# Kernel optimization log

Hardware: AMD Instinct MI355X
Metric: run time of the kernel (lower is better)

The kernel has to match this reference:

```python
import jax, jax.numpy as jnp
import numpy as np

N_NODES = 20000
N_EDGES = 200000
D_MODEL = 128
N_HEADS = 8
N_LAYERS = 2  # num_gnn - 1 concat layers


def setup_inputs() -> dict:
    key = jax.random.key(0)
    ks = jax.random.split(key, 12)
    s = 0.05  # keep activations well-scaled across residual layers
    hd = D_MODEL // N_HEADS  # 16
    return {
        "x": jax.random.normal(ks[0], (N_NODES, D_MODEL), jnp.float32),
        "src": jax.random.randint(ks[1], (N_EDGES,), 0, N_NODES),
        "dst": jax.random.randint(ks[2], (N_EDGES,), 0, N_NODES),
        "Ws": jax.random.normal(ks[3], (N_LAYERS, D_MODEL, D_MODEL), jnp.float32) * s,
        "als": jax.random.normal(ks[4], (N_LAYERS, N_HEADS, hd), jnp.float32) * s,
        "ars": jax.random.normal(ks[5], (N_LAYERS, N_HEADS, hd), jnp.float32) * s,
        "bs": jax.random.normal(ks[6], (N_LAYERS, D_MODEL), jnp.float32) * s,
        "W_last": jax.random.normal(ks[7], (D_MODEL, N_HEADS * D_MODEL), jnp.float32) * s,
        "al_last": jax.random.normal(ks[8], (N_HEADS, D_MODEL), jnp.float32) * s,
        "ar_last": jax.random.normal(ks[9], (N_HEADS, D_MODEL), jnp.float32) * s,
        "b_last": jax.random.normal(ks[10], (N_HEADS * D_MODEL,), jnp.float32) * s,
    }


def gat_conv(h, src, dst, W, al, ar, b, num_nodes):
    """DGL GATConv (eval mode, dropout off): returns (N, H, D) head outputs."""
    H, D = al.shape
    feat = (h @ W).reshape(num_nodes, H, D)          # (N,H,D)
    el = jnp.sum(feat * al[None], axis=-1)           # (N,H) attn on src side
    er = jnp.sum(feat * ar[None], axis=-1)           # (N,H) attn on dst side
    e = jax.nn.leaky_relu(el[src] + er[dst], 0.2)    # (E,H)
    # edge softmax over incoming edges of each dst node, per head
    m = jax.ops.segment_max(e, dst, num_segments=num_nodes)  # (N,H)
    p = jnp.exp(e - m[dst])                          # (E,H)
    z = jax.ops.segment_sum(p, dst, num_segments=num_nodes)  # (N,H)
    a = p / z[dst]                                   # (E,H)
    msg = feat[src] * a[..., None]                   # (E,H,D) weighted messages
    rst = jax.ops.segment_sum(msg, dst, num_segments=num_nodes)  # (N,H,D)
    return rst + b.reshape(1, H, D)


def reference(x, src, dst, Ws, als, ars, bs, W_last, al_last, ar_last, b_last):
    N = x.shape[0]
    h = x
    for i in range(N_LAYERS):
        temp = gat_conv(h, src, dst, Ws[i], als[i], ars[i], bs[i], N)  # (N,H,hd)
        h = h + jax.nn.elu(temp.reshape(N, -1))       # concat heads, ELU, residual
    temp = gat_conv(h, src, dst, W_last, al_last, ar_last, b_last, N)  # (N,H,D)
    h = h + jnp.mean(temp, axis=1)                    # mean over heads, residual
    return h
```

## Files before the change

### kernel.cpp

```cpp
#include <hip/hip_runtime.h>
#include <math.h>

#define N_NODES 20000
#define N_EDGES 200000
#define DM 128
#define NH 8

typedef __attribute__((ext_vector_type(8))) short bf16x8;
typedef __attribute__((ext_vector_type(4))) float f32x4;

__device__ __forceinline__ unsigned short f2b(float f) {
  unsigned int u = __float_as_uint(f);
  unsigned int r = (u + 0x7FFFu + ((u >> 16) & 1u)) >> 16;
  return (unsigned short)r;
}
__device__ __forceinline__ float b2f(unsigned short s) {
  return __uint_as_float(((unsigned int)s) << 16);
}

__global__ __launch_bounds__(256) void degzero(int* __restrict__ deg) {
  int i = blockIdx.x * 256 + threadIdx.x;
  if (i < N_NODES) deg[i] = 0;
}

__global__ __launch_bounds__(256) void prep_all(
    const float* __restrict__ x, float* __restrict__ h, unsigned short* __restrict__ hb,
    const int* __restrict__ dstE, int* __restrict__ deg, int* __restrict__ rank,
    const float* __restrict__ Ws, unsigned short* __restrict__ wsz,
    const float* __restrict__ W_last, unsigned short* __restrict__ wpsz,
    const float* __restrict__ al_last, const float* __restrict__ ar_last,
    const float* __restrict__ b_last, unsigned short* __restrict__ wlrsz,
    float* __restrict__ mb) {
  int i = blockIdx.x * 256 + threadIdx.x;
  if (i < (N_NODES * DM) / 4) {
    float4 v = ((const float4*)x)[i];
    ((float4*)h)[i] = v;
    ((ushort4*)hb)[i] = make_ushort4(f2b(v.x), f2b(v.y), f2b(v.z), f2b(v.w));
  }
  if (i < N_EDGES) rank[i] = atomicAdd(&deg[dstE[i]], 1);
  if (i < 2 * 16384) {
    int layer = i >> 14;
    int r = i & 16383;
    int j = r & 7, l = (r >> 3) & 63, f = (r >> 9) & 7, ks = r >> 12;
    int k = ks * 32 + ((l >> 4) << 3) + j;
    int n = f * 16 + (l & 15);
    wsz[i] = f2b(Ws[(size_t)layer * 16384 + k * 128 + n]);
  }
  if (i < 131072) {
    int j = i & 7, l = (i >> 3) & 63, f = (i >> 9) & 7, ks = i >> 12;
    int k = ks * 32 + ((l >> 4) << 3) + j;
    int n = f * 16 + (l & 15);
    int h_ = k >> 7, ko = k & 127;
    wpsz[i] = f2b(W_last[(size_t)ko * 1024 + h_ * 128 + n] * 0.125f);
  }
  if (i < 2048) {
    int j = i & 7, l = (i >> 3) & 63, ks = i >> 9;
    int k = ks * 32 + ((l >> 4) << 3) + j;
    int n = l & 15;
    int hh = n & 7;
    const float* av = (n < 8) ? (al_last + hh * 128) : (ar_last + hh * 128);
    float s = 0.f;
    for (int d = 0; d < 128; ++d) s += W_last[(size_t)k * 1024 + hh * 128 + d] * av[d];
    wlrsz[i] = f2b(s);
  }
  if (i < 128) {
    float s = 0.f;
#pragma unroll
    for (int hh = 0; hh < 8; ++hh) s += b_last[hh * 128 + i];
    mb[i] = s * 0.125f;
  }
}

__global__ void scan_deg(const int* __restrict__ deg, int* __restrict__ off,
                         int* __restrict__ bbase_g, int* __restrict__ bcur_g) {
  __shared__ int part[1024];
  __shared__ int hist[16][64];
  const int tid = threadIdx.x;
  const int wv = tid >> 6, lane = tid & 63;
  const int CHUNK = (N_NODES + 1023) / 1024;
  int base = tid * CHUNK;

  for (int i = tid; i < 16 * 64; i += 1024) ((int*)hist)[i] = 0;
  __syncthreads();

  int s = 0;
  for (int i = 0; i < CHUNK; ++i) {
    int idx = base + i;
    if (idx < N_NODES) {
      int d = deg[idx];
      s += d;
      atomicAdd(&hist[wv][min(d, 63)], 1);
    }
  }
  part[tid] = s;
  __syncthreads();
  for (int ofs = 1; ofs < 1024; ofs <<= 1) {
    int v = (tid >= ofs) ? part[tid - ofs] : 0;
    __syncthreads();
    part[tid] += v;
    __syncthreads();
  }
  int run = (tid > 0) ? part[tid - 1] : 0;
  for (int i = 0; i < CHUNK; ++i) {
    int idx = base + i;
    if (idx < N_NODES) {
      off[idx] = run;
      run += deg[idx];
    }
  }
  if (tid == 0) off[N_NODES] = part[1023];

  if (wv == 0) {
    int c = 0;
#pragma unroll
    for (int w = 0; w < 16; ++w) c += hist[w][lane];
    int inc = c;
#pragma unroll
    for (int ofs = 1; ofs < 64; ofs <<= 1) {
      int v = __shfl_up(inc, ofs, 64);
      if (lane >= ofs) inc += v;
    }
    bbase_g[lane] = inc - c;
    bcur_g[lane] = 0;
  }
}

template <int K>
__device__ __forceinline__ void dev_gemm(int tile, const unsigned short* __restrict__ A,
                                         const unsigned short* __restrict__ Bsz,
                                         unsigned short* __restrict__ Cb,
                                         const float* __restrict__ al,
                                         const float* __restrict__ ar,
                                         float* __restrict__ elr, int lane, int wid) {
  const int wrow = wid & 1, wc = wid >> 1;
  const int r0 = tile * 32;
  const int arow = r0 + wrow * 16 + (lane & 15);
  const int kg = lane >> 4;

  f32x4 acc[4];
#pragma unroll
  for (int fi = 0; fi < 4; ++fi) acc[fi] = {0.f, 0.f, 0.f, 0.f};

  const bf16x8* Ap = (const bf16x8*)(A + (size_t)arow * K + kg * 8);
#pragma unroll 4
  for (int ks = 0; ks < K / 32; ++ks) {
    bf16x8 a = Ap[ks * 4];
#pragma unroll
    for (int fi = 0; fi < 4; ++fi) {
      int f = wc * 4 + fi;
      bf16x8 b = *(const bf16x8*)(Bsz + (((size_t)(ks * 8 + f) * 64 + lane) << 3));
      acc[fi] = __builtin_amdgcn_mfma_f32_16x16x32_bf16(a, b, acc[fi], 0, 0, 0);
    }
  }

  const int rbase = r0 + wrow * 16 + (lane >> 4) * 4;
#pragma unroll
  for (int fi = 0; fi < 4; ++fi) {
    int col = wc * 64 + fi * 16 + (lane & 15);
#pragma unroll
    for (int r = 0; r < 4; ++r) {
      Cb[(size_t)(rbase + r) * DM + col] = f2b(acc[fi][r]);
    }
  }

#pragma unroll
  for (int fi = 0; fi < 4; ++fi) {
    int hh = wc * 4 + fi;
    float alv = al[hh * 16 + (lane & 15)];
    float arv = ar[hh * 16 + (lane & 15)];
#pragma unroll
    for (int r = 0; r < 4; ++r) {
      float pl = acc[fi][r] * alv;
      float pr = acc[fi][r] * arv;
#pragma unroll
      for (int msk = 1; msk < 16; msk <<= 1) {
        pl += __shfl_xor(pl, msk, 64);
        pr += __shfl_xor(pr, msk, 64);
      }
      if ((lane & 15) == 0) {
        int row = rbase + r;
        elr[row * 16 + hh] = pl;
        elr[row * 16 + 8 + hh] = pr;
      }
    }
  }
}

__global__ __launch_bounds__(256) void gemm0_scatter(
    const unsigned short* __restrict__ A, const unsigned short* __restrict__ Bsz,
    unsigned short* __restrict__ Cb, const float* __restrict__ al,
    const float* __restrict__ ar, float* __restrict__ elr, const int* __restrict__ srcE,
    const int* __restrict__ dstE, const int* __restrict__ rank,
    const int* __restrict__ off, int* __restrict__ csr_src, const int* __restrict__ deg,
    const int* __restrict__ bbase_g, int* __restrict__ bcur_g, int* __restrict__ perm) {
  __shared__ int lcnt[64];
  __shared__ int gbase[64];
  const int bid = blockIdx.x;
  const int GB = N_NODES / 32;
  const int EB = (N_EDGES + 255) / 256;
  if (bid < GB) {
    dev_gemm<DM>(bid, A, Bsz, Cb, al, ar, elr, threadIdx.x & 63, threadIdx.x >> 6);
  } else if (bid < GB + EB) {
    int e = (bid - GB) * 256 + threadIdx.x;
    if (e < N_EDGES) {
      csr_src[off[dstE[e]] + rank[e]] = srcE[e];
    }
  } else {
    const int tid = threadIdx.x;
    int idx = (bid - GB - EB) * 256 + tid;
    if (tid < 64) lcnt[tid] = 0;
    __syncthreads();
    int d = 0, lrank = 0;
    bool valid = idx < N_NODES;
    if (valid) {
      d = min(deg[idx], 63);
      lrank = atomicAdd(&lcnt[d], 1);
    }
    __syncthreads();
    if (tid < 64 && lcnt[tid] > 0) gbase[tid] = atomicAdd(&bcur_g[tid], lcnt[tid]);
    __syncthreads();
    if (valid) perm[bbase_g[d] + gbase[d] + lrank] = idx;
  }
}

template <int MODE>
__global__ __launch_bounds__(256) void fused_small(
    const int* __restrict__ perm, const int* __restrict__ off,
    const int* __restrict__ csr_src, const unsigned short* __restrict__ feat,
    const float* __restrict__ elr, const float* __restrict__ bias, float* __restrict__ h,
    unsigned short* __restrict__ hb, const unsigned short* __restrict__ wsz1,
    const float* __restrict__ al1, const float* __restrict__ ar1,
    unsigned short* __restrict__ feat_out, float* __restrict__ elr_out,
    const unsigned short* __restrict__ wlrsz, float* __restrict__ elr2_out) {
  __shared__ float a_lds[4][64];
  __shared__ int s_lds[4][8];
  __shared__ float zi_lds[4][8];
  __shared__ __align__(16) unsigned short nh_lds[4][128];
  __shared__ int pnode[4];
  const int wid = threadIdx.x >> 6;
  const int t = perm[blockIdx.x * 4 + wid];
  const int lane = threadIdx.x & 63;
  const int e_loc = lane >> 3, hh = lane & 7;
  const int hg = lane >> 3;
  const int beg = off[t], end = off[t + 1];
  const float ert = elr[t * 16 + 8 + hh];
  if (lane == 0) pnode[wid] = t;

  int e = beg + e_loc;
  bool val = e < end;
  int s = val ? csr_src[e] : 0;
  float xl = val ? elr[s * 16 + hh] : 0.f;

  float z = 0.f, acc0 = 0.f, acc1 = 0.f;
  for (int base = beg; base < end; base += 8) {
    float ex = 0.f;
    if (val) {
      float xv = xl + ert;
      xv = xv > 0.f ? xv : 0.2f * xv;
      ex = __expf(xv);
    }
    a_lds[wid][lane] = ex;
    if (hh == 0) s_lds[wid][e_loc] = s;
    __builtin_amdgcn_wave_barrier();
    asm volatile("s_waitcnt lgkmcnt(0)" ::: "memory");
    z += ex;
    int en = base + 8 + e_loc;
    bool valn = en < end;
    int sn = valn ? csr_src[en] : 0;
    float xln = valn ? elr[sn * 16 + hh] : 0.f;
    int n = min(8, end - base);
    if (n == 8) {
#pragma unroll
      for (int e2 = 0; e2 < 8; ++e2) {
        int s2 = s_lds[wid][e2];
        float a = a_lds[wid][e2 * 8 + hg];
        unsigned int hv = *(const unsigned int*)&feat[(size_t)s2 * 128 + 2 * lane];
        acc0 += a * b2f((unsigned short)(hv & 0xffffu));
        acc1 += a * b2f((unsigned short)(hv >> 16));
      }
    } else {
      for (int e2 = 0; e2 < n; ++e2) {
        int s2 = s_lds[wid][e2];
        float a = a_lds[wid][e2 * 8 + hg];
        unsigned int hv = *(const unsigned int*)&feat[(size_t)s2 * 128 + 2 * lane];
        acc0 += a * b2f((unsigned short)(hv & 0xffffu));
        acc1 += a * b2f((unsigned short)(hv >> 16));
      }
    }
    __builtin_amdgcn_wave_barrier();
    s = sn;
    xl = xln;
    val = valn;
  }
  z += __shfl_xor(z, 8, 64);
  z += __shfl_xor(z, 16, 64);
  z += __shfl_xor(z, 32, 64);
  if (e_loc == 0) zi_lds[wid][hh] = (z > 0.f) ? 1.f / z : 0.f;
  __builtin_amdgcn_wave_barrier();
  asm volatile("s_waitcnt lgkmcnt(0)" ::: "memory");
  float zi = zi_lds[wid][hg];

  float2 bv = *(const float2*)&bias[2 * lane];
  float v0 = acc0 * zi + bv.x;
  float v1 = acc1 * zi + bv.y;
  v0 = v0 > 0.f ? v0 : expm1f(v0);
  v1 = v1 > 0.f ? v1 : expm1f(v1);
  size_t idx = (size_t)t * 128 + 2 * lane;
  float2 hv = *(const float2*)&h[idx];
  float nh0 = hv.x + v0;
  float nh1 = hv.y + v1;
  *(float2*)&h[idx] = make_float2(nh0, nh1);
  unsigned short b0 = f2b(nh0), b1 = f2b(nh1);
  *(ushort2*)&hb[idx] = make_ushort2(b0, b1);
  *(ushort2*)&nh_lds[wid][2 * lane] = make_ushort2(b0, b1);

  if (MODE == 1) {
    __builtin_amdgcn_wave_barrier();
    asm volatile("s_waitcnt lgkmcnt(0)" ::: "memory");
    const int kg = lane >> 4;
    f32x4 acc = {0.f, 0.f, 0.f, 0.f};
#pragma unroll
    for (int ks = 0; ks < 4; ++ks) {
      bf16x8 a = *(const bf16x8*)&nh_lds[wid][ks * 32 + kg * 8];
      bf16x8 b = *(const bf16x8*)(wlrsz + (((size_t)ks * 64 + lane) << 3));
      acc = __builtin_amdgcn_mfma_f32_16x16x32_bf16(a, b, acc, 0, 0, 0);
    }
    if (lane < 16) elr2_out[t * 16 + lane] = acc[0];
  }

  if (MODE == 0) {
    __syncthreads();
    const int r16 = lane & 15;
    const int kg = lane >> 4;
    f32x4 acc2[2];
    acc2[0] = {0.f, 0.f, 0.f, 0.f};
    acc2[1] = {0.f, 0.f, 0.f, 0.f};
#pragma unroll
    for (int ks = 0; ks < 4; ++ks) {
      bf16x8 a = {0, 0, 0, 0, 0, 0, 0, 0};
      if (r16 < 4) a = *(const bf16x8*)&nh_lds[r16][ks * 32 + kg * 8];
#pragma unroll
      for (int fi = 0; fi < 2; ++fi) {
        int f = wid * 2 + fi;
        bf16x8 b = *(const bf16x8*)(wsz1 + (((size_t)(ks * 8 + f) * 64 + lane) << 3));
        acc2[fi] = __builtin_amdgcn_mfma_f32_16x16x32_bf16(a, b, acc2[fi], 0, 0, 0);
      }
    }
    const int rowl = (lane >> 4) * 4;
#pragma unroll
    for (int fi = 0; fi < 2; ++fi) {
      int f = wid * 2 + fi;
      int col = f * 16 + r16;
      float alv = al1[col];
      float arv = ar1[col];
#pragma unroll
      for (int r = 0; r < 4; ++r) {
        float v = acc2[fi][r];
        if (rowl == 0) feat_out[(size_t)pnode[r] * 128 + col] = f2b(v);
        float pl = v * alv;
        float pr = v * arv;
#pragma unroll
        for (int msk = 1; msk < 16; msk <<= 1) {
          pl += __shfl_xor(pl, msk, 64);
          pr += __shfl_xor(pr, msk, 64);
        }
        if (r16 == 0 && rowl == 0) {
          int pn = pnode[r];
          elr_out[pn * 16 + f] = pl;
          elr_out[pn * 16 + 8 + f] = pr;
        }
      }
    }
  }
}

#define GT_STRIDE 1032
__global__ __launch_bounds__(1024) void agg_gemm16(
    const int* __restrict__ perm, const int* __restrict__ off,
    const int* __restrict__ csr_src, const unsigned short* __restrict__ hb,
    const float* __restrict__ elr, const unsigned short* __restrict__ wpsz,
    const float* __restrict__ hres, const float* __restrict__ mb,
    float* __restrict__ out) {
  __shared__ __align__(16) unsigned short gt[16][GT_STRIDE];
  __shared__ float red[8][64][4];
  __shared__ float a_lds[16][64];
  __shared__ int s_lds[16][8];
  __shared__ float zi_lds[16][8];
  __shared__ int pnode[16];
  const int wid = threadIdx.x >> 6;
  const int lane = threadIdx.x & 63;
  const int t0 = blockIdx.x * 16;
  const int t = perm[t0 + wid];
  const int e_loc = lane >> 3, hh = lane & 7;
  if (lane == 0) pnode[wid] = t;

  {
    const int beg = off[t], end = off[t + 1];
    const float ert = elr[t * 16 + 8 + hh];
    int e = beg + e_loc;
    bool val = e < end;
    int s = val ? csr_src[e] : 0;
    float xl = val ? elr[s * 16 + hh] : 0.f;

    float z = 0.f;
    float accA[8], accB[8];
#pragma unroll
    for (int k = 0; k < 8; ++k) accA[k] = accB[k] = 0.f;

    for (int base = beg; base < end; base += 8) {
      float ex = 0.f;
      if (val) {
        float xv = xl + ert;
        xv = xv > 0.f ? xv : 0.2f * xv;
        ex = __expf(xv);
      }
      a_lds[wid][lane] = ex;
      if (hh == 0) s_lds[wid][e_loc] = s;
      __builtin_amdgcn_wave_barrier();
      asm volatile("s_waitcnt lgkmcnt(0)" ::: "memory");
      z += ex;
      int en = base + 8 + e_loc;
      bool valn = en < end;
      int sn = valn ? csr_src[en] : 0;
      float xln = valn ? elr[sn * 16 + hh] : 0.f;
      int n = min(8, end - base);
      if (n == 8) {
#pragma unroll
        for (int e2 = 0; e2 < 8; ++e2) {
          int s2 = s_lds[wid][e2];
          float4 pa = *(const float4*)&a_lds[wid][e2 * 8];
          float4 pb = *(const float4*)&a_lds[wid][e2 * 8 + 4];
          unsigned int hv = *(const unsigned int*)&hb[(size_t)s2 * 128 + 2 * lane];
          float h0 = b2f((unsigned short)(hv & 0xffffu));
          float h1 = b2f((unsigned short)(hv >> 16));
          accA[0] += pa.x * h0; accB[0] += pa.x * h1;
          accA[1] += pa.y * h0; accB[1] += pa.y * h1;
          accA[2] += pa.z * h0; accB[2] += pa.z * h1;
          accA[3] += pa.w * h0; accB[3] += pa.w * h1;
          accA[4] += pb.x * h0; accB[4] += pb.x * h1;
          accA[5] += pb.y * h0; accB[5] += pb.y * h1;
          accA[6] += pb.z * h0; accB[6] += pb.z * h1;
          accA[7] += pb.w * h0; accB[7] += pb.w * h1;
        }
      } else {
        for (int e2 = 0; e2 < n; ++e2) {
          int s2 = s_lds[wid][e2];
          float4 pa = *(const float4*)&a_lds[wid][e2 * 8];
          float4 pb = *(const float4*)&a_lds[wid][e2 * 8 + 4];
          unsigned int hv = *(const unsigned int*)&hb[(size_t)s2 * 128 + 2 * lane];
          float h0 = b2f((unsigned short)(hv & 0xffffu));
          float h1 = b2f((unsigned short)(hv >> 16));
          accA[0] += pa.x * h0; accB[0] += pa.x * h1;
          accA[1] += pa.y * h0; accB[1] += pa.y * h1;
          accA[2] += pa.z * h0; accB[2] += pa.z * h1;
          accA[3] += pa.w * h0; accB[3] += pa.w * h1;
          accA[4] += pb.x * h0; accB[4] += pb.x * h1;
          accA[5] += pb.y * h0; accB[5] += pb.y * h1;
          accA[6] += pb.z * h0; accB[6] += pb.z * h1;
          accA[7] += pb.w * h0; accB[7] += pb.w * h1;
        }
      }
      __builtin_amdgcn_wave_barrier();
      s = sn;
      xl = xln;
      val = valn;
    }
    z += __shfl_xor(z, 8, 64);
    z += __shfl_xor(z, 16, 64);
    z += __shfl_xor(z, 32, 64);
    if (e_loc == 0) zi_lds[wid][hh] = (z > 0.f) ? 1.f / z : 0.f;
    __builtin_amdgcn_wave_barrier();
    asm volatile("s_waitcnt lgkmcnt(0)" ::: "memory");
    float4 zia = *(const float4*)&zi_lds[wid][0];
    float4 zib = *(const float4*)&zi_lds[wid][4];
    float ziv[8] = {zia.x, zia.y, zia.z, zia.w, zib.x, zib.y, zib.z, zib.w};
#pragma unroll
    for (int h2 = 0; h2 < 8; ++h2) {
      *(ushort2*)&gt[wid][h2 * 128 + 2 * lane] =
          make_ushort2(f2b(accA[h2] * ziv[h2]), f2b(accB[h2] * ziv[h2]));
    }
  }
  __syncthreads();

  const int f = wid & 7;
  const int kh = wid >> 3;
  const int ar16 = lane & 15;
  const int kg = lane >> 4;
  f32x4 acc = {0.f, 0.f, 0.f, 0.f};
#pragma unroll 4
  for (int ksl = 0; ksl < 16; ++ksl) {
    int ks = kh * 16 + ksl;
    bf16x8 a = *(const bf16x8*)&gt[ar16][ks * 32 + kg * 8];
    bf16x8 b = *(const bf16x8*)(wpsz + (((size_t)(ks * 8 + f) * 64 + lane) << 3));
    acc = __builtin_amdgcn_mfma_f32_16x16x32_bf16(a, b, acc, 0, 0, 0);
  }
  if (kh == 1) {
    *(float4*)&red[f][lane][0] = make_float4(acc[0], acc[1], acc[2], acc[3]);
  }
  __syncthreads();
  if (kh == 0) {
    float4 p = *(const float4*)&red[f][lane][0];
    const int col = f * 16 + (lane & 15);
    const int rb = (lane >> 4) * 4;
    float r4[4] = {p.x, p.y, p.z, p.w};
#pragma unroll
    for (int r = 0; r < 4; ++r) {
      int row = pnode[rb + r];
      out[(size_t)row * 128 + col] =
          acc[r] + r4[r] + hres[(size_t)row * 128 + col] + mb[col];
    }
  }
}

extern "C" void kernel_launch(void* const* d_in, const int* in_sizes, int n_in,
                              void* d_out, int out_size, void* d_ws, size_t ws_size,
                              hipStream_t stream) {
  const float* x = (const float*)d_in[0];
  const int* src = (const int*)d_in[1];
  const int* dst = (const int*)d_in[2];
  const float* Ws = (const float*)d_in[3];
  const float* als = (const float*)d_in[4];
  const float* ars = (const float*)d_in[5];
  const float* bs = (const float*)d_in[6];
  const float* W_last = (const float*)d_in[7];
  const float* al_last = (const float*)d_in[8];
  const float* ar_last = (const float*)d_in[9];
  const float* b_last = (const float*)d_in[10];
  float* out = (float*)d_out;

  float* h = (float*)d_ws;
  float* elr0 = h + 2560000;
  float* elrB = elr0 + 320000;
  float* elr2 = elrB + 320000;
  float* mb = elr2 + 320000;
  unsigned short* hb = (unsigned short*)(mb + 128);
  unsigned short* featA = hb + 2560000;
  unsigned short* featB = featA + 2560000;
  unsigned short* wsz = featB + 2560000;
  unsigned short* wpsz = wsz + 32768;
  unsigned short* wlrsz = wpsz + 131072;
  int* deg = (int*)(wlrsz + 2048);
  int* off = deg + N_NODES;
  int* rank = off + N_NODES + 1;
  int* csr_src = rank + N_EDGES;
  int* perm = csr_src + N_EDGES;
  int* bbase_g = perm + N_NODES;
  int* bcur_g = bbase_g + 64;

  const int GB = N_NODES / 32;
  const int FB = N_NODES / 4;
  const int EB = (N_EDGES + 255) / 256;
  const int PB = (N_NODES + 255) / 256;

  degzero<<<(N_NODES + 255) / 256, 256, 0, stream>>>(deg);
  prep_all<<<(N_NODES * DM / 4 + 255) / 256, 256, 0, stream>>>(
      x, h, hb, dst, deg, rank, Ws, wsz, W_last, wpsz, al_last, ar_last, b_last, wlrsz, mb);
  scan_deg<<<1, 1024, 0, stream>>>(deg, off, bbase_g, bcur_g);
  gemm0_scatter<<<GB + EB + PB, 256, 0, stream>>>(hb, wsz, featA, als, ars, elr0, src,
                                                  dst, rank, off, csr_src, deg, bbase_g,
                                                  bcur_g, perm);
  fused_small<0><<<FB, 256, 0, stream>>>(perm, off, csr_src, featA, elr0, bs, h, hb,
                                         wsz + 16384, als + 128, ars + 128, featB, elrB,
                                         nullptr, nullptr);
  fused_small<1><<<FB, 256, 0, stream>>>(perm, off, csr_src, featB, elrB, bs + 128, h, hb,
                                         nullptr, nullptr, nullptr, nullptr, nullptr,
                                         wlrsz, elr2);
  agg_gemm16<<<N_NODES / 16, 1024, 0, stream>>>(perm, off, csr_src, hb, elr2, wpsz, h, mb,
                                                out);
}
```

Measured before the change: 161.5 us.

## Overlap degree scan with first GEMM and prefetch neighbor features in final aggregation

The single-block degree scan now runs as an extra 256-thread block inside the layer-0 GEMM launch, so it overlaps the GEMM instead of running alone as a serial 1024-thread kernel. The CSR scatter and degree-bucket permutation move into their own kernel that follows. In the final aggregation kernel, the neighbor bf16 feature loads are software-pipelined one chunk of eight edges ahead, with source indices broadcast via shuffles instead of LDS. The edge indices and logits are also prefetched two chunks ahead. This hides gather latency at the cost of extra registers and one more kernel launch.

```diff
diff --git a/kernel.cpp b/kernel.cpp
--- a/kernel.cpp
+++ b/kernel.cpp
@@ -71,60 +71,6 @@
   }
 }
 
-__global__ void scan_deg(const int* __restrict__ deg, int* __restrict__ off,
-                         int* __restrict__ bbase_g, int* __restrict__ bcur_g) {
-  __shared__ int part[1024];
-  __shared__ int hist[16][64];
-  const int tid = threadIdx.x;
-  const int wv = tid >> 6, lane = tid & 63;
-  const int CHUNK = (N_NODES + 1023) / 1024;
-  int base = tid * CHUNK;
-
-  for (int i = tid; i < 16 * 64; i += 1024) ((int*)hist)[i] = 0;
-  __syncthreads();
-
-  int s = 0;
-  for (int i = 0; i < CHUNK; ++i) {
-    int idx = base + i;
-    if (idx < N_NODES) {
-      int d = deg[idx];
-      s += d;
-      atomicAdd(&hist[wv][min(d, 63)], 1);
-    }
-  }
-  part[tid] = s;
-  __syncthreads();
-  for (int ofs = 1; ofs < 1024; ofs <<= 1) {
-    int v = (tid >= ofs) ? part[tid - ofs] : 0;
-    __syncthreads();
-    part[tid] += v;
-    __syncthreads();
-  }
-  int run = (tid > 0) ? part[tid - 1] : 0;
-  for (int i = 0; i < CHUNK; ++i) {
-    int idx = base + i;
-    if (idx < N_NODES) {
-      off[idx] = run;
-      run += deg[idx];
-    }
-  }
-  if (tid == 0) off[N_NODES] = part[1023];
-
-  if (wv == 0) {
-    int c = 0;
-#pragma unroll
-    for (int w = 0; w < 16; ++w) c += hist[w][lane];
-    int inc = c;
-#pragma unroll
-    for (int ofs = 1; ofs < 64; ofs <<= 1) {
-      int v = __shfl_up(inc, ofs, 64);
-      if (lane >= ofs) inc += v;
-    }
-    bbase_g[lane] = inc - c;
-    bcur_g[lane] = 0;
-  }
-}
-
 template <int K>
 __device__ __forceinline__ void dev_gemm(int tile, const unsigned short* __restrict__ A,
                                          const unsigned short* __restrict__ Bsz,
@@ -186,28 +132,76 @@
   }
 }
 
-__global__ __launch_bounds__(256) void gemm0_scatter(
+__global__ __launch_bounds__(256) void gemm0_scan(
     const unsigned short* __restrict__ A, const unsigned short* __restrict__ Bsz,
     unsigned short* __restrict__ Cb, const float* __restrict__ al,
-    const float* __restrict__ ar, float* __restrict__ elr, const int* __restrict__ srcE,
-    const int* __restrict__ dstE, const int* __restrict__ rank,
-    const int* __restrict__ off, int* __restrict__ csr_src, const int* __restrict__ deg,
-    const int* __restrict__ bbase_g, int* __restrict__ bcur_g, int* __restrict__ perm) {
+    const float* __restrict__ ar, float* __restrict__ elr, const int* __restrict__ deg,
+    int* __restrict__ off, int* __restrict__ bbase_g, int* __restrict__ bcur_g) {
+  const int bid = blockIdx.x;
+  const int GB = N_NODES / 32;
+  if (bid < GB) {
+    dev_gemm<DM>(bid, A, Bsz, Cb, al, ar, elr, threadIdx.x & 63, threadIdx.x >> 6);
+    return;
+  }
+  __shared__ int part[256];
+  __shared__ int hist[4][64];
+  const int tid = threadIdx.x;
+  const int wv = tid >> 6, lane = tid & 63;
+  const int CHUNK = (N_NODES + 255) / 256;
+  const int b0 = tid * CHUNK;
+  const int b1 = min(N_NODES, b0 + CHUNK);
+  if (tid < 64) {
+    hist[0][tid] = 0; hist[1][tid] = 0; hist[2][tid] = 0; hist[3][tid] = 0;
+  }
+  __syncthreads();
+  int s = 0;
+  for (int idx = b0; idx < b1; ++idx) {
+    int d = deg[idx];
+    s += d;
+    atomicAdd(&hist[wv][min(d, 63)], 1);
+  }
+  part[tid] = s;
+  __syncthreads();
+  for (int ofs = 1; ofs < 256; ofs <<= 1) {
+    int v = (tid >= ofs) ? part[tid - ofs] : 0;
+    __syncthreads();
+    part[tid] += v;
+    __syncthreads();
+  }
+  int run = (tid > 0) ? part[tid - 1] : 0;
+  for (int idx = b0; idx < b1; ++idx) {
+    off[idx] = run;
+    run += deg[idx];
+  }
+  if (tid == 255) off[N_NODES] = part[255];
+  if (wv == 0) {
+    int c = hist[0][lane] + hist[1][lane] + hist[2][lane] + hist[3][lane];
+    int inc = c;
+#pragma unroll
+    for (int ofs = 1; ofs < 64; ofs <<= 1) {
+      int v = __shfl_up(inc, ofs, 64);
+      if (lane >= ofs) inc += v;
+    }
+    bbase_g[lane] = inc - c;
+    bcur_g[lane] = 0;
+  }
+}
+
+__global__ __launch_bounds__(256) void scatter_both(
+    const int* __restrict__ srcE, const int* __restrict__ dstE,
+    const int* __restrict__ rank, const int* __restrict__ off, int* __restrict__ csr_src,
+    const int* __restrict__ deg, const int* __restrict__ bbase_g,
+    int* __restrict__ bcur_g, int* __restrict__ perm) {
   __shared__ int lcnt[64];
   __shared__ int gbase[64];
   const int bid = blockIdx.x;
-  const int GB = N_NODES / 32;
   const int EB = (N_EDGES + 255) / 256;
-  if (bid < GB) {
-    dev_gemm<DM>(bid, A, Bsz, Cb, al, ar, elr, threadIdx.x & 63, threadIdx.x >> 6);
-  } else if (bid < GB + EB) {
-    int e = (bid - GB) * 256 + threadIdx.x;
-    if (e < N_EDGES) {
-      csr_src[off[dstE[e]] + rank[e]] = srcE[e];
-    }
+  if (bid < EB) {
+    int e = bid * 256 + threadIdx.x;
+    if (e < N_EDGES) csr_src[off[dstE[e]] + rank[e]] = srcE[e];
   } else {
     const int tid = threadIdx.x;
-    int idx = (bid - GB - EB) * 256 + tid;
+    int idx = (bid - EB) * 256 + tid;
     if (tid < 64) lcnt[tid] = 0;
     __syncthreads();
     int d = 0, lrank = 0;
@@ -384,7 +378,6 @@
   __shared__ __align__(16) unsigned short gt[16][GT_STRIDE];
   __shared__ float red[8][64][4];
   __shared__ float a_lds[16][64];
-  __shared__ int s_lds[16][8];
   __shared__ float zi_lds[16][8];
   __shared__ int pnode[16];
   const int wid = threadIdx.x >> 6;
@@ -397,10 +390,28 @@
   {
     const int beg = off[t], end = off[t + 1];
     const float ert = elr[t * 16 + 8 + hh];
-    int e = beg + e_loc;
-    bool val = e < end;
-    int s = val ? csr_src[e] : 0;
-    float xl = val ? elr[s * 16 + hh] : 0.f;
+
+    int eA = beg + e_loc;
+    bool vA = eA < end;
+    int sA = vA ? csr_src[eA] : 0;
+    float xA = vA ? elr[sA * 16 + hh] : 0.f;
+    int eB = beg + 8 + e_loc;
+    bool vB = eB < end;
+    int sB = vB ? csr_src[eB] : 0;
+    float xB = vB ? elr[sB * 16 + hh] : 0.f;
+
+    unsigned int hvc[8];
+    {
+      int n0 = end - beg;
+      if (n0 > 8) n0 = 8;
+#pragma unroll
+      for (int e2 = 0; e2 < 8; ++e2) {
+        if (e2 < n0) {
+          int s2 = __shfl(sA, e2 * 8, 64);
+          hvc[e2] = *(const unsigned int*)&hb[(size_t)s2 * 128 + 2 * lane];
+        }
+      }
+    }
 
     float z = 0.f;
     float accA[8], accB[8];
@@ -409,30 +420,40 @@
 
     for (int base = beg; base < end; base += 8) {
       float ex = 0.f;
-      if (val) {
-        float xv = xl + ert;
+      if (vA) {
+        float xv = xA + ert;
         xv = xv > 0.f ? xv : 0.2f * xv;
         ex = __expf(xv);
       }
       a_lds[wid][lane] = ex;
-      if (hh == 0) s_lds[wid][e_loc] = s;
       __builtin_amdgcn_wave_barrier();
       asm volatile("s_waitcnt lgkmcnt(0)" ::: "memory");
       z += ex;
-      int en = base + 8 + e_loc;
-      bool valn = en < end;
-      int sn = valn ? csr_src[en] : 0;
-      float xln = valn ? elr[sn * 16 + hh] : 0.f;
-      int n = min(8, end - base);
-      if (n == 8) {
-#pragma unroll
-        for (int e2 = 0; e2 < 8; ++e2) {
-          int s2 = s_lds[wid][e2];
+
+      unsigned int hvn[8];
+      int n1 = end - base - 8;
+      if (n1 > 8) n1 = 8;
+#pragma unroll
+      for (int e2 = 0; e2 < 8; ++e2) {
+        if (e2 < n1) {
+          int s2 = __shfl(sB, e2 * 8, 64);
+          hvn[e2] = *(const unsigned int*)&hb[(size_t)s2 * 128 + 2 * lane];
+        }
+      }
+      int eC = base + 16 + e_loc;
+      bool vC = eC < end;
+      int sC = vC ? csr_src[eC] : 0;
+      float xC = vC ? elr[sC * 16 + hh] : 0.f;
+
+      int n = end - base;
+      if (n > 8) n = 8;
+#pragma unroll
+      for (int e2 = 0; e2 < 8; ++e2) {
+        if (e2 < n) {
           float4 pa = *(const float4*)&a_lds[wid][e2 * 8];
           float4 pb = *(const float4*)&a_lds[wid][e2 * 8 + 4];
-          unsigned int hv = *(const unsigned int*)&hb[(size_t)s2 * 128 + 2 * lane];
-          float h0 = b2f((unsigned short)(hv & 0xffffu));
-          float h1 = b2f((unsigned short)(hv >> 16));
+          float h0 = b2f((unsigned short)(hvc[e2] & 0xffffu));
+          float h1 = b2f((unsigned short)(hvc[e2] >> 16));
           accA[0] += pa.x * h0; accB[0] += pa.x * h1;
           accA[1] += pa.y * h0; accB[1] += pa.y * h1;
           accA[2] += pa.z * h0; accB[2] += pa.z * h1;
@@ -442,28 +463,12 @@
           accA[6] += pb.z * h0; accB[6] += pb.z * h1;
           accA[7] += pb.w * h0; accB[7] += pb.w * h1;
         }
-      } else {
-        for (int e2 = 0; e2 < n; ++e2) {
-          int s2 = s_lds[wid][e2];
-          float4 pa = *(const float4*)&a_lds[wid][e2 * 8];
-          float4 pb = *(const float4*)&a_lds[wid][e2 * 8 + 4];
-          unsigned int hv = *(const unsigned int*)&hb[(size_t)s2 * 128 + 2 * lane];
-          float h0 = b2f((unsigned short)(hv & 0xffffu));
-          float h1 = b2f((unsigned short)(hv >> 16));
-          accA[0] += pa.x * h0; accB[0] += pa.x * h1;
-          accA[1] += pa.y * h0; accB[1] += pa.y * h1;
-          accA[2] += pa.z * h0; accB[2] += pa.z * h1;
-          accA[3] += pa.w * h0; accB[3] += pa.w * h1;
-          accA[4] += pb.x * h0; accB[4] += pb.x * h1;
-          accA[5] += pb.y * h0; accB[5] += pb.y * h1;
-          accA[6] += pb.z * h0; accB[6] += pb.z * h1;
-          accA[7] += pb.w * h0; accB[7] += pb.w * h1;
-        }
       }
       __builtin_amdgcn_wave_barrier();
-      s = sn;
-      xl = xln;
-      val = valn;
+#pragma unroll
+      for (int e2 = 0; e2 < 8; ++e2) hvc[e2] = hvn[e2];
+      sA = sB; xA = xB; vA = vB;
+      sB = sC; xB = xC; vB = vC;
     }
     z += __shfl_xor(z, 8, 64);
     z += __shfl_xor(z, 16, 64);
@@ -555,10 +560,10 @@
   degzero<<<(N_NODES + 255) / 256, 256, 0, stream>>>(deg);
   prep_all<<<(N_NODES * DM / 4 + 255) / 256, 256, 0, stream>>>(
       x, h, hb, dst, deg, rank, Ws, wsz, W_last, wpsz, al_last, ar_last, b_last, wlrsz, mb);
-  scan_deg<<<1, 1024, 0, stream>>>(deg, off, bbase_g, bcur_g);
-  gemm0_scatter<<<GB + EB + PB, 256, 0, stream>>>(hb, wsz, featA, als, ars, elr0, src,
-                                                  dst, rank, off, csr_src, deg, bbase_g,
-                                                  bcur_g, perm);
+  gemm0_scan<<<GB + 1, 256, 0, stream>>>(hb, wsz, featA, als, ars, elr0, deg, off,
+                                         bbase_g, bcur_g);
+  scatter_both<<<EB + PB, 256, 0, stream>>>(src, dst, rank, off, csr_src, deg, bbase_g,
+                                            bcur_g, perm);
   fused_small<0><<<FB, 256, 0, stream>>>(perm, off, csr_src, featA, elr0, bs, h, hb,
                                          wsz + 16384, als + 128, ars + 128, featB, elrB,
                                          nullptr, nullptr);
```

Result: slower. 176.3 us (+9.2%).
